# Kernel optimization log

Hardware: AMD Instinct MI355X
Metric: run time of the kernel (lower is better)

The kernel has to match this reference:

```python
import jax, jax.numpy as jnp
import numpy as np

N, C, E = 4096, 128, 10          # nodes, channels, element types
LMAX = 2
NI = (LMAX + 1) ** 2             # 9 spherical components of node_feats
K = {1: 4, 2: 12, 3: 30}         # number of CG paths per correlation order
DIMS = [2 * L + 1 for L in range(LMAX + 1)]  # output irrep dims [1,3,5]


def setup_inputs() -> dict:
    key = jax.random.key(0)
    ks = iter(jax.random.split(key, 64))
    inp = {}
    inp["node_feats"] = jax.random.normal(next(ks), (N, C, NI), jnp.float32)
    inp["sc"] = jax.random.normal(next(ks), (N, C * sum(DIMS)), jnp.float32)
    z = jax.random.randint(next(ks), (N,), 0, E)
    inp["node_attrs"] = jax.nn.one_hot(z, E, dtype=jnp.float32)
    for L, d in enumerate(DIMS):
        # U tensors: fixed Clebsch-Gordan-structured constants (stand-in values,
        # correct shapes/contraction pattern of MACE's U_matrix buffers).
        inp[f"U3_L{L}"] = jax.random.normal(next(ks), (d, NI, NI, NI, K[3]), jnp.float32) * 0.05
        inp[f"U2_L{L}"] = jax.random.normal(next(ks), (d, NI, NI, K[2]), jnp.float32) * 0.05
        inp[f"U1_L{L}"] = jax.random.normal(next(ks), (d, NI, K[1]), jnp.float32) * 0.05
        # Element-dependent path weights [num_elements, k, channels]
        inp[f"W3_L{L}"] = jax.random.normal(next(ks), (E, K[3], C), jnp.float32) / np.sqrt(K[3])
        inp[f"W2_L{L}"] = jax.random.normal(next(ks), (E, K[2], C), jnp.float32) / np.sqrt(K[2])
        inp[f"W1_L{L}"] = jax.random.normal(next(ks), (E, K[1], C), jnp.float32) / np.sqrt(K[1])
        # o3.Linear channel-mixing weight for this irrep
        inp[f"lin_L{L}"] = jax.random.normal(next(ks), (C, C), jnp.float32)
    return inp


def _contract(x, y, U3, U2, U1, W3, W2, W1):
    """MACE symmetric contraction (correlation=3) for one output irrep.
    x: [b,c,n] node feats, y: [b,e] one-hot element attrs.
    Recursive einsum structure from mace.modules.symmetric_contraction.Contraction."""
    out = jnp.einsum('dijnk,ekc,bcn,be->bcdij', U3, W3, x, y)
    c2 = jnp.einsum('dijk,ekc,be->bcdij', U2, W2, y) + out
    out = jnp.einsum('bcdij,bcj->bcdi', c2, x)
    c1 = jnp.einsum('dik,ekc,be->bcdi', U1, W1, y) + out
    return jnp.einsum('bcdi,bci->bcd', c1, x)  # [b,c,d]


def reference(node_feats, sc, node_attrs,
              U3_L0, U2_L0, U1_L0, W3_L0, W2_L0, W1_L0, lin_L0,
              U3_L1, U2_L1, U1_L1, W3_L1, W2_L1, W1_L1, lin_L1,
              U3_L2, U2_L2, U1_L2, W3_L2, W2_L2, W1_L2, lin_L2):
    Us = [(U3_L0, U2_L0, U1_L0), (U3_L1, U2_L1, U1_L1), (U3_L2, U2_L2, U1_L2)]
    Ws = [(W3_L0, W2_L0, W1_L0), (W3_L1, W2_L1, W1_L1), (W3_L2, W2_L2, W1_L2)]
    lins = [lin_L0, lin_L1, lin_L2]
    c = node_feats.shape[1]
    norm = jnp.asarray(1.0 / np.sqrt(c), node_feats.dtype)
    outs = []
    for (u3, u2, u1), (w3, w2, w1), lw in zip(Us, Ws, lins):
        o = _contract(node_feats, node_attrs, u3, u2, u1, w3, w2, w1)  # [b,c,d]
        o = jnp.einsum('bcd,cf->bfd', o, lw) * norm                    # o3.Linear mix
        outs.append(o.reshape(o.shape[0], -1))
    return jnp.concatenate(outs, axis=-1) + sc
```

## Files before the change

### kernel.cpp

```cpp
#include <hip/hip_runtime.h>

#define NNODES 4096
#define NCH    128
#define NE     10
#define PADN   4736
#define NCHUNK 74
#define TSTRIDE 2048
#define DGSTRIDE 672


struct MTab { unsigned short v[220]; };
static constexpr MTab make_mtab() {
    MTab t{};
    int m = 0;
    for (int i = 0; i < 9; ++i) {
        t.v[m++] = (unsigned short)((1 << 12) | (i << 8) | (i << 4) | i);
        for (int j = i; j < 9; ++j) {
            t.v[m++] = (unsigned short)((2 << 12) | (i << 8) | (j << 4) | j);
            for (int n = j; n < 9; ++n)
                t.v[m++] = (unsigned short)((3 << 12) | (i << 8) | (j << 4) | n);
        }
    }
    return t;
}
__constant__ MTab c_mtab = make_mtab();

__global__ __launch_bounds__(1024) void k_prep(
    const float* __restrict__ attrs,
    const float* __restrict__ U3_0, const float* __restrict__ U3_1, const float* __restrict__ U3_2,
    const float* __restrict__ W3_0, const float* __restrict__ W3_1, const float* __restrict__ W3_2,
    const float* __restrict__ U2_0, const float* __restrict__ U2_1, const float* __restrict__ U2_2,
    const float* __restrict__ W2_0, const float* __restrict__ W2_1, const float* __restrict__ W2_2,
    const float* __restrict__ U1_0, const float* __restrict__ U1_1, const float* __restrict__ U1_2,
    const float* __restrict__ W1_0, const float* __restrict__ W1_1, const float* __restrict__ W1_2,
    int* __restrict__ list, int* __restrict__ chunkinfo,
    float* __restrict__ wcat, float* __restrict__ Usym)
{
    int bid = blockIdx.x, t = threadIdx.x;
    if (bid == 0) {
        __shared__ int cnt[64][NE];
        __shared__ int pfx[64][NE];
        __shared__ int tot[NE];
        __shared__ int base[NE + 1], cbase[NE + 1];
        int w = t >> 6, lane = t & 63;
        unsigned long long lmask = (1ull << lane) - 1ull;
        int mye[4];
#pragma unroll
        for (int k = 0; k < 4; ++k) {
            int b = k * 1024 + t;
            const float* y = attrs + (size_t)b * NE;
            int e = 0;
#pragma unroll
            for (int u = 0; u < NE; ++u) if (y[u] > 0.5f) e = u;
            mye[k] = e;
#pragma unroll
            for (int u = 0; u < NE; ++u) {
                unsigned long long mb = __ballot(e == u);
                if (lane == 0) cnt[w * 4 + k][u] = __popcll(mb);
            }
        }
        for (int i = t; i < PADN; i += 1024) list[i] = -1;
        __syncthreads();
        if (t < 640) {
            int e = t >> 6, wi = t & 63;
            int v = cnt[wi][e];
            int inc = v;
#pragma unroll
            for (int d = 1; d < 64; d <<= 1) {
                int o = __shfl_up(inc, d, 64);
                if (wi >= d) inc += o;
            }
            pfx[wi][e] = inc - v;
            if (wi == 63) tot[e] = inc;
        }
        __syncthreads();
        if (t == 0) {
            int off = 0, goff = 0;
            for (int e = 0; e < NE; ++e) {
                base[e] = off; cbase[e] = goff;
                int nc = (tot[e] + 63) >> 6;
                off += nc * 64; goff += nc;
            }
            base[NE] = off; cbase[NE] = goff;
        }
        __syncthreads();
        if (t < 80) {
            int info = -1;
            if (t < cbase[NE]) {
                int e = 0;
                while (!(t >= cbase[e] && t < cbase[e + 1])) ++e;
                int k = t - cbase[e];
                int valid = tot[e] - k * 64; if (valid > 64) valid = 64;
                info = (base[e] + k * 64) | (valid << 16) | (e << 24);
            }
            chunkinfo[t] = info;
        } else if (t < 91) {
            chunkinfo[t] = cbase[t - 80];
        }
#pragma unroll
        for (int k = 0; k < 4; ++k) {
            int e = mye[k];
#pragma unroll
            for (int u = 0; u < NE; ++u) {
                unsigned long long mb = __ballot(e == u);
                if (e == u) {
                    int pos = base[u] + pfx[w * 4 + k][u] + __popcll(mb & lmask);
                    list[pos] = k * 1024 + t;
                }
            }
        }
    } else if (bid <= 10) {
        int e = bid - 1;
#pragma unroll 1
        for (int L = 0; L < 3; ++L) {
            const float* W1 = (L == 0) ? W1_0 : (L == 1) ? W1_1 : W1_2;
            const float* W2 = (L == 0) ? W2_0 : (L == 1) ? W2_1 : W2_2;
            const float* W3 = (L == 0) ? W3_0 : (L == 1) ? W3_1 : W3_2;
            for (int it = t; it < 48 * 128; it += 1024) {
                int c = it & 127, k = it >> 7;
                float v = 0.0f;
                if (k < 4)       v = W1[((size_t)e * 4 + k) * 128 + c];
                else if (k < 16) v = W2[((size_t)e * 12 + (k - 4)) * 128 + c];
                else if (k < 46) v = W3[((size_t)e * 30 + (k - 16)) * 128 + c];
                wcat[(((size_t)L * NE + e) * 48 + k) * 128 + c] = v;
            }
        }
    } else {
        int D = bid - 11;
        const float *U3, *U2, *U1; int dloc;
        if (D == 0)      { U3 = U3_0; U2 = U2_0; U1 = U1_0; dloc = 0; }
        else if (D < 4)  { U3 = U3_1; U2 = U2_1; U1 = U1_1; dloc = D - 1; }
        else             { U3 = U3_2; U2 = U2_2; U1 = U1_2; dloc = D - 4; }
        for (int it = t; it < 219 * 48; it += 1024) {
            int m = it / 48, k = it - m * 48;
            unsigned mv = c_mtab.v[m];
            int kind = mv >> 12, i = (mv >> 8) & 15, j = (mv >> 4) & 15, n = mv & 15;
            float v = 0.0f;
            if (kind == 1) {
                if (k < 4) v = U1[(size_t)(dloc * 9 + i) * 4 + k];
            } else if (kind == 2) {
                if (k >= 4 && k < 16) {
                    int kk = k - 4;
                    v = U2[(size_t)(dloc * 81 + i * 9 + j) * 12 + kk];
                    if (i != j) v += U2[(size_t)(dloc * 81 + j * 9 + i) * 12 + kk];
                }
            } else {
                if (k >= 16 && k < 46) {
                    int kk = k - 16;
                    v = U3[((size_t)dloc * 729 + i * 81 + j * 9 + n) * 30 + kk];
                    if (i == j) {
                        if (j != n)
                            v += U3[((size_t)dloc * 729 + i * 81 + n * 9 + i) * 30 + kk]
                               + U3[((size_t)dloc * 729 + n * 81 + i * 9 + i) * 30 + kk];
                    } else if (j == n) {
                        v += U3[((size_t)dloc * 729 + j * 81 + i * 9 + j) * 30 + kk]
                           + U3[((size_t)dloc * 729 + j * 81 + j * 9 + i) * 30 + kk];
                    } else {
                        v += U3[((size_t)dloc * 729 + i * 81 + n * 9 + j) * 30 + kk]
                           + U3[((size_t)dloc * 729 + j * 81 + i * 9 + n) * 30 + kk]
                           + U3[((size_t)dloc * 729 + j * 81 + n * 9 + i) * 30 + kk]
                           + U3[((size_t)dloc * 729 + n * 81 + i * 9 + j) * 30 + kk]
                           + U3[((size_t)dloc * 729 + n * 81 + j * 9 + i) * 30 + kk];
                    }
                }
            }
            Usym[((size_t)D * 219 + m) * 48 + k] = v;
        }
    }
}

__global__ __launch_bounds__(256) void k_tab(
    const float* __restrict__ wcat, const float* __restrict__ Usym,
    float* __restrict__ Sws)
{
    __shared__ __align__(16) float tile[84 * 129];
    int bid = blockIdx.x;
    int e = bid / 24, r0 = bid - e * 24;
    int dg = r0 >> 3, mh = r0 & 7;
    int m0 = mh * 28, m1 = m0 + 28; if (m1 > 219) m1 = 219;
    int t = threadIdx.x;
    int c = t & 127;
    int sub = __builtin_amdgcn_readfirstlane(t >> 7);
    int D0 = dg * 3;
    int LA = (D0 == 0) ? 0 : (D0 < 4 ? 1 : 2);
    int LB = (D0 + 1 < 4) ? 1 : 2;

    float wcA[48], wcB[48];
#pragma unroll
    for (int k = 0; k < 48; ++k) {
        wcA[k] = wcat[(((size_t)LA * NE + e) * 48 + k) * 128 + c];
        wcB[k] = wcat[(((size_t)LB * NE + e) * 48 + k) * 128 + c];
    }

#pragma unroll 1
    for (int m = m0 + sub; m < m1; m += 2) {
        unsigned mv = c_mtab.v[m];
        int kind = mv >> 12;
        const float* up0 = Usym + ((size_t)D0 * 219 + m) * 48;
        const float* up1 = up0 + 219 * 48;
        const float* up2 = up1 + 219 * 48;
        float a0 = 0.0f, a1 = 0.0f, a2 = 0.0f;
        if (kind == 1) {
#pragma unroll
            for (int k = 0; k < 4; ++k) {
                a0 = fmaf(up0[k], wcA[k], a0);
                a1 = fmaf(up1[k], wcB[k], a1);
                a2 = fmaf(up2[k], wcB[k], a2);
            }
        } else if (kind == 2) {
#pragma unroll
            for (int k = 4; k < 16; ++k) {
                a0 = fmaf(up0[k], wcA[k], a0);
                a1 = fmaf(up1[k], wcB[k], a1);
                a2 = fmaf(up2[k], wcB[k], a2);
            }
        } else {
#pragma unroll
            for (int k = 16; k < 46; ++k) {
                a0 = fmaf(up0[k], wcA[k], a0);
                a1 = fmaf(up1[k], wcB[k], a1);
                a2 = fmaf(up2[k], wcB[k], a2);
            }
        }
        int rr = (m - m0) * 3;
        tile[(rr + 0) * 129 + c] = a0;
        tile[(rr + 1) * 129 + c] = a1;
        tile[(rr + 2) * 129 + c] = a2;
    }
    __syncthreads();

    int w = t >> 6, lane = t & 63;
    int nrows = (m1 - m0) * 3;
#pragma unroll 1
    for (int cc = 0; cc < 32; ++cc) {
        int co = w * 32 + cc;
        float* op = Sws + ((size_t)e * NCH + co) * TSTRIDE + dg * DGSTRIDE + m0 * 3;
#pragma unroll
        for (int rr = lane; rr < 84; rr += 64)
            if (rr < nrows) op[rr] = tile[rr * 129 + co];
    }
}

template <int NB>
__device__ __forceinline__ void do_chunks(
    const float* __restrict__ tab, const float* __restrict__ nf,
    const int* __restrict__ list, const int* __restrict__ chunkinfo,
    float* __restrict__ prep, int c, int gi, int lane)
{
    int pos[NB];
    float x[NB][9];
#pragma unroll
    for (int u = 0; u < NB; ++u) {
        int info = __builtin_amdgcn_readfirstlane(chunkinfo[gi + u]);
        pos[u] = (info & 0xffff) + lane;
        int b = list[pos[u]];
        const float* xp = nf + ((size_t)(b < 0 ? 0 : b) * 128 + c) * 9;
#pragma unroll
        for (int n = 0; n < 9; ++n) x[u][n] = (b >= 0) ? xp[n] : 0.0f;
    }

#pragma unroll 1
    for (int dg = 0; dg < 3; ++dg) {
        const float* s = tab + dg * DGSTRIDE;
        float a3[NB][3];
#pragma unroll
        for (int u = 0; u < NB; ++u)
#pragma unroll
            for (int d = 0; d < 3; ++d) a3[u][d] = 0.0f;
        int p = 0;
#pragma unroll
        for (int i = 0; i < 9; ++i) {
            float a2[NB][3];
#pragma unroll
            for (int d = 0; d < 3; ++d) {
                float tv = s[p + d];
#pragma unroll
                for (int u = 0; u < NB; ++u) a2[u][d] = tv;
            }
            p += 3;
#pragma unroll
            for (int j = i; j < 9; ++j) {
                float a1[NB][3];
#pragma unroll
                for (int d = 0; d < 3; ++d) {
                    float tv = s[p + d];
#pragma unroll
                    for (int u = 0; u < NB; ++u) a1[u][d] = tv;
                }
                p += 3;
#pragma unroll
                for (int n = j; n < 9; ++n) {
#pragma unroll
                    for (int d = 0; d < 3; ++d) {
                        float tv = s[p + d];
#pragma unroll
                        for (int u = 0; u < NB; ++u)
                            a1[u][d] = fmaf(tv, x[u][n], a1[u][d]);
                    }
                    p += 3;
                }
#pragma unroll
                for (int u = 0; u < NB; ++u)
#pragma unroll
                    for (int d = 0; d < 3; ++d)
                        a2[u][d] = fmaf(a1[u][d], x[u][j], a2[u][d]);
            }
#pragma unroll
            for (int u = 0; u < NB; ++u)
#pragma unroll
                for (int d = 0; d < 3; ++d)
                    a3[u][d] = fmaf(a2[u][d], x[u][i], a3[u][d]);
        }
#pragma unroll
        for (int u = 0; u < NB; ++u)
#pragma unroll
            for (int d = 0; d < 3; ++d)
                prep[(size_t)(dg * 3 + d) * PADN + pos[u]] = a3[u][d];
    }
}

__global__ __launch_bounds__(256) void k_main(
    const float* __restrict__ nf, const int* __restrict__ list,
    const int* __restrict__ chunkinfo, const float* __restrict__ Sws,
    float* __restrict__ pre)
{
    __shared__ __align__(16) float tab[TSTRIDE];
    int c = blockIdx.x, e = blockIdx.y;
    int t = threadIdx.x;
    int w = t >> 6, lane = t & 63;
    int cb0 = chunkinfo[80 + e], cb1 = chunkinfo[81 + e];
    if (cb0 >= cb1) return;

    {
        const float4* src = (const float4*)(Sws + ((size_t)e * NCH + c) * TSTRIDE);
        float4* dst = (float4*)tab;
        dst[t] = src[t];
        dst[t + 256] = src[t + 256];
    }
    __syncthreads();

    float* prep = pre + (size_t)c * 9 * PADN;

#pragma unroll 1
    for (int gi = cb0 + 2 * w; gi < cb1; gi += 8) {
        if (gi + 1 < cb1)
            do_chunks<2>(tab, nf, list, chunkinfo, prep, c, gi, lane);
        else
            do_chunks<1>(tab, nf, list, chunkinfo, prep, c, gi, lane);
    }
}

__global__ __launch_bounds__(256) void k_mix(
    const float* __restrict__ pre, const int* __restrict__ chunkinfo,
    const float* __restrict__ lin0, const float* __restrict__ lin1,
    const float* __restrict__ lin2, float* __restrict__ mixed)
{
    __shared__ __align__(16) float pt[128 * 64];
    int bid = blockIdx.x;
    int nt = bid >> 1;
    int fbase = (bid & 1) * 64;
    int n0 = nt * 64;
    int D = nt / NCHUNK;
    int g = nt - D * NCHUNK;
    if (chunkinfo[g] == -1) return;
    const float* lin = (D == 0) ? lin0 : (D < 4 ? lin1 : lin2);
    int t = threadIdx.x;

    {
        int q4 = (t & 15) * 4;
        int cb = t >> 4;
#pragma unroll
        for (int k = 0; k < 8; ++k) {
            int c = cb + k * 16;
            float4 v = *(const float4*)&pre[(size_t)c * 9 * PADN + n0 + q4];
            *(float4*)&pt[c * 64 + q4] = v;
        }
    }
    __syncthreads();

    int tq = t & 63;
    int f0 = fbase + __builtin_amdgcn_readfirstlane(t >> 6) * 16;
    float acc[16];
#pragma unroll
    for (int f = 0; f < 16; ++f) acc[f] = 0.0f;

#pragma unroll 4
    for (int c = 0; c < 128; ++c) {
        float pv = pt[c * 64 + tq];
        const float* lr = lin + c * 128 + f0;
#pragma unroll
        for (int f = 0; f < 16; ++f)
            acc[f] = fmaf(pv, lr[f], acc[f]);
    }

    const float nrm = 0.08838834764831845f;
#pragma unroll
    for (int f = 0; f < 16; ++f)
        mixed[(size_t)(f0 + f) * 9 * PADN + n0 + tq] = acc[f] * nrm;
}

__global__ __launch_bounds__(256) void k_out(
    const float* __restrict__ mixed, const int* __restrict__ list,
    const int* __restrict__ chunkinfo, const float* __restrict__ sc,
    float* __restrict__ out)
{
    __shared__ float tr[64 * 73];
    int fc = blockIdx.x, g = blockIdx.y;
    if (chunkinfo[g] == -1) return;
    int t = threadIdx.x;
    int fbase = fc * 8;
    int tf = t >> 6, tq = t & 63;

#pragma unroll
    for (int k = 0; k < 18; ++k) {
        int row = k * 4 + tf;
        int f = row / 9, D = row - f * 9;
        float v = mixed[((size_t)(fbase + f) * 9 + D) * PADN + g * 64 + tq];
        tr[tq * 73 + row] = v;
    }
    __syncthreads();

#pragma unroll 1
    for (int k = 0; k < 18; ++k) {
        int idx = k * 256 + t;
        int node = idx / 72, col = idx - node * 72;
        int b = list[g * 64 + node];
        if (b < 0) continue;
        int row, gcol;
        if (col < 8)       { row = col * 9;                       gcol = fbase + col; }
        else if (col < 32) { int u = col - 8;  int f = u / 3, dl = u - f * 3;
                             row = f * 9 + 1 + dl;                gcol = 128 + fbase * 3 + u; }
        else               { int u = col - 32; int f = u / 5, dl = u - f * 5;
                             row = f * 9 + 4 + dl;                gcol = 512 + fbase * 5 + u; }
        out[(size_t)b * 1152 + gcol] = tr[node * 73 + row] + sc[(size_t)b * 1152 + gcol];
    }
}

extern "C" void kernel_launch(void* const* d_in, const int* in_sizes, int n_in,
                              void* d_out, int out_size, void* d_ws, size_t ws_size,
                              hipStream_t stream)
{
    const float* nf    = (const float*)d_in[0];
    const float* sc    = (const float*)d_in[1];
    const float* attrs = (const float*)d_in[2];
    const float *U3s[3], *U2s[3], *U1s[3], *W3s[3], *W2s[3], *W1s[3], *lins[3];
    for (int L = 0; L < 3; ++L) {
        const int o = 3 + 7 * L;
        U3s[L]  = (const float*)d_in[o + 0];
        U2s[L]  = (const float*)d_in[o + 1];
        U1s[L]  = (const float*)d_in[o + 2];
        W3s[L]  = (const float*)d_in[o + 3];
        W2s[L]  = (const float*)d_in[o + 4];
        W1s[L]  = (const float*)d_in[o + 5];
        lins[L] = (const float*)d_in[o + 6];
    }

    float* wsf     = (float*)d_ws;
    int* chunkinfo = (int*)d_ws;
    int* list      = chunkinfo + 96;
    float* Sws   = wsf + 4864;
    float* pre   = Sws + (size_t)NE * NCH * TSTRIDE;
    float* mixed = pre + (size_t)NCH * 9 * PADN;
    float* wcat  = mixed + (size_t)NCH * 9 * PADN;
    float* Usym  = wcat + (size_t)3 * NE * 48 * 128;

    k_prep<<<20, 1024, 0, stream>>>(attrs,
                                    U3s[0], U3s[1], U3s[2], W3s[0], W3s[1], W3s[2],
                                    U2s[0], U2s[1], U2s[2], W2s[0], W2s[1], W2s[2],
                                    U1s[0], U1s[1], U1s[2], W1s[0], W1s[1], W1s[2],
                                    list, chunkinfo, wcat, Usym);
    k_tab<<<240, 256, 0, stream>>>(wcat, Usym, Sws);
    k_main<<<dim3(128, 10), 256, 0, stream>>>(nf, list, chunkinfo, Sws, pre);
    k_mix<<<1332, 256, 0, stream>>>(pre, chunkinfo, lins[0], lins[1], lins[2], mixed);
    k_out<<<dim3(16, NCHUNK), 256, 0, stream>>>(mixed, list, chunkinfo, sc, (float*)d_out);
}
```

Before: 241.7 us.

## Fuse per-channel table construction into main kernel and drop k_tab

Removes the separate k_tab launch and its global Sws table. Each k_main block now builds its own per-(element, channel) table in shared memory by contracting Usym with a transposed wcat, whose new channel-major layout keeps a channel's 48 weights contiguous. This saves a kernel launch and a large global write and read round-trip. In exchange the table work is redone inside every block, using strided, uncoalesced global reads with little register reuse.

Result: slower. 260.9 us (+7.9%).

```diff
diff --git a/kernel.cpp b/kernel.cpp
--- a/kernel.cpp
+++ b/kernel.cpp
@@ -116,13 +116,13 @@
             const float* W1 = (L == 0) ? W1_0 : (L == 1) ? W1_1 : W1_2;
             const float* W2 = (L == 0) ? W2_0 : (L == 1) ? W2_1 : W2_2;
             const float* W3 = (L == 0) ? W3_0 : (L == 1) ? W3_1 : W3_2;
-            for (int it = t; it < 48 * 128; it += 1024) {
-                int c = it & 127, k = it >> 7;
+            for (int it = t; it < 128 * 48; it += 1024) {
+                int c = it / 48, k = it - c * 48;
                 float v = 0.0f;
                 if (k < 4)       v = W1[((size_t)e * 4 + k) * 128 + c];
                 else if (k < 16) v = W2[((size_t)e * 12 + (k - 4)) * 128 + c];
                 else if (k < 46) v = W3[((size_t)e * 30 + (k - 16)) * 128 + c];
-                wcat[(((size_t)L * NE + e) * 48 + k) * 128 + c] = v;
+                wcat[(((size_t)L * NE + e) * 128) * 48 + it] = v;
             }
         }
     } else {
@@ -169,78 +169,6 @@
     }
 }
 
-__global__ __launch_bounds__(256) void k_tab(
-    const float* __restrict__ wcat, const float* __restrict__ Usym,
-    float* __restrict__ Sws)
-{
-    __shared__ __align__(16) float tile[84 * 129];
-    int bid = blockIdx.x;
-    int e = bid / 24, r0 = bid - e * 24;
-    int dg = r0 >> 3, mh = r0 & 7;
-    int m0 = mh * 28, m1 = m0 + 28; if (m1 > 219) m1 = 219;
-    int t = threadIdx.x;
-    int c = t & 127;
-    int sub = __builtin_amdgcn_readfirstlane(t >> 7);
-    int D0 = dg * 3;
-    int LA = (D0 == 0) ? 0 : (D0 < 4 ? 1 : 2);
-    int LB = (D0 + 1 < 4) ? 1 : 2;
-
-    float wcA[48], wcB[48];
-#pragma unroll
-    for (int k = 0; k < 48; ++k) {
-        wcA[k] = wcat[(((size_t)LA * NE + e) * 48 + k) * 128 + c];
-        wcB[k] = wcat[(((size_t)LB * NE + e) * 48 + k) * 128 + c];
-    }
-
-#pragma unroll 1
-    for (int m = m0 + sub; m < m1; m += 2) {
-        unsigned mv = c_mtab.v[m];
-        int kind = mv >> 12;
-        const float* up0 = Usym + ((size_t)D0 * 219 + m) * 48;
-        const float* up1 = up0 + 219 * 48;
-        const float* up2 = up1 + 219 * 48;
-        float a0 = 0.0f, a1 = 0.0f, a2 = 0.0f;
-        if (kind == 1) {
-#pragma unroll
-            for (int k = 0; k < 4; ++k) {
-                a0 = fmaf(up0[k], wcA[k], a0);
-                a1 = fmaf(up1[k], wcB[k], a1);
-                a2 = fmaf(up2[k], wcB[k], a2);
-            }
-        } else if (kind == 2) {
-#pragma unroll
-            for (int k = 4; k < 16; ++k) {
-                a0 = fmaf(up0[k], wcA[k], a0);
-                a1 = fmaf(up1[k], wcB[k], a1);
-                a2 = fmaf(up2[k], wcB[k], a2);
-            }
-        } else {
-#pragma unroll
-            for (int k = 16; k < 46; ++k) {
-                a0 = fmaf(up0[k], wcA[k], a0);
-                a1 = fmaf(up1[k], wcB[k], a1);
-                a2 = fmaf(up2[k], wcB[k], a2);
-            }
-        }
-        int rr = (m - m0) * 3;
-        tile[(rr + 0) * 129 + c] = a0;
-        tile[(rr + 1) * 129 + c] = a1;
-        tile[(rr + 2) * 129 + c] = a2;
-    }
-    __syncthreads();
-
-    int w = t >> 6, lane = t & 63;
-    int nrows = (m1 - m0) * 3;
-#pragma unroll 1
-    for (int cc = 0; cc < 32; ++cc) {
-        int co = w * 32 + cc;
-        float* op = Sws + ((size_t)e * NCH + co) * TSTRIDE + dg * DGSTRIDE + m0 * 3;
-#pragma unroll
-        for (int rr = lane; rr < 84; rr += 64)
-            if (rr < nrows) op[rr] = tile[rr * 129 + co];
-    }
-}
-
 template <int NB>
 __device__ __forceinline__ void do_chunks(
     const float* __restrict__ tab, const float* __restrict__ nf,
@@ -321,8 +249,8 @@
 
 __global__ __launch_bounds__(256) void k_main(
     const float* __restrict__ nf, const int* __restrict__ list,
-    const int* __restrict__ chunkinfo, const float* __restrict__ Sws,
-    float* __restrict__ pre)
+    const int* __restrict__ chunkinfo, const float* __restrict__ wcat,
+    const float* __restrict__ Usym, float* __restrict__ pre)
 {
     __shared__ __align__(16) float tab[TSTRIDE];
     int c = blockIdx.x, e = blockIdx.y;
@@ -331,11 +259,28 @@
     int cb0 = chunkinfo[80 + e], cb1 = chunkinfo[81 + e];
     if (cb0 >= cb1) return;
 
-    {
-        const float4* src = (const float4*)(Sws + ((size_t)e * NCH + c) * TSTRIDE);
-        float4* dst = (float4*)tab;
-        dst[t] = src[t];
-        dst[t + 256] = src[t + 256];
+#pragma unroll 1
+    for (int idx = t; idx < 1971; idx += 256) {
+        int dg = idx / 657, r = idx - dg * 657;
+        int m = r / 3, dr = r - m * 3;
+        int D = dg * 3 + dr;
+        int L = (D == 0) ? 0 : (D < 4 ? 1 : 2);
+        const float* wc = wcat + (((size_t)L * NE + e) * 128 + c) * 48;
+        const float* up = Usym + ((size_t)D * 219 + m) * 48;
+        unsigned mv = c_mtab.v[m];
+        int kind = mv >> 12;
+        float a = 0.0f;
+        if (kind == 1) {
+#pragma unroll
+            for (int k = 0; k < 4; ++k) a = fmaf(up[k], wc[k], a);
+        } else if (kind == 2) {
+#pragma unroll
+            for (int k = 4; k < 16; ++k) a = fmaf(up[k], wc[k], a);
+        } else {
+#pragma unroll
+            for (int k = 16; k < 46; ++k) a = fmaf(up[k], wc[k], a);
+        }
+        tab[dg * DGSTRIDE + m * 3 + dr] = a;
     }
     __syncthreads();
 
@@ -458,19 +403,17 @@
     float* wsf     = (float*)d_ws;
     int* chunkinfo = (int*)d_ws;
     int* list      = chunkinfo + 96;
-    float* Sws   = wsf + 4864;
-    float* pre   = Sws + (size_t)NE * NCH * TSTRIDE;
+    float* pre   = wsf + 4864;
     float* mixed = pre + (size_t)NCH * 9 * PADN;
     float* wcat  = mixed + (size_t)NCH * 9 * PADN;
-    float* Usym  = wcat + (size_t)3 * NE * 48 * 128;
+    float* Usym  = wcat + (size_t)3 * NE * 128 * 48;
 
     k_prep<<<20, 1024, 0, stream>>>(attrs,
                                     U3s[0], U3s[1], U3s[2], W3s[0], W3s[1], W3s[2],
                                     U2s[0], U2s[1], U2s[2], W2s[0], W2s[1], W2s[2],
                                     U1s[0], U1s[1], U1s[2], W1s[0], W1s[1], W1s[2],
                                     list, chunkinfo, wcat, Usym);
-    k_tab<<<240, 256, 0, stream>>>(wcat, Usym, Sws);
-    k_main<<<dim3(128, 10), 256, 0, stream>>>(nf, list, chunkinfo, Sws, pre);
+    k_main<<<dim3(128, 10), 256, 0, stream>>>(nf, list, chunkinfo, wcat, Usym, pre);
     k_mix<<<1332, 256, 0, stream>>>(pre, chunkinfo, lins[0], lins[1], lins[2], mixed);
     k_out<<<dim3(16, NCHUNK), 256, 0, stream>>>(mixed, list, chunkinfo, sc, (float*)d_out);
 }
```
